# Performance work log

Hardware: AMD Instinct MI355X
Metric: run time of the kernel (lower is better)

## Reference

```python
import jax, jax.numpy as jnp
import numpy as np

B, N, D, H = 64, 1025, 768, 128

def setup_inputs() -> dict:
    key = jax.random.key(0)
    ks = jax.random.split(key, 5)
    x = jax.random.normal(ks[0], (B, N, D), dtype=jnp.float32)
    ln_w = jnp.ones((D,), dtype=jnp.float32)
    ln_b = jnp.zeros((D,), dtype=jnp.float32)
    w1 = jax.random.normal(ks[1], (D, H), dtype=jnp.float32) * (1.0 / np.sqrt(D))
    b1 = jnp.zeros((H,), dtype=jnp.float32)
    w2 = jax.random.normal(ks[2], (H, 1), dtype=jnp.float32) * (1.0 / np.sqrt(H))
    b2 = jnp.zeros((1,), dtype=jnp.float32)
    return {"x": x, "ln_w": ln_w, "ln_b": ln_b, "w1": w1, "b1": b1, "w2": w2, "b2": b2, "k": 256}

def _layernorm(x, w, b, eps=1e-5):
    mu = jnp.mean(x, axis=-1, keepdims=True)
    var = jnp.mean(jnp.square(x - mu), axis=-1, keepdims=True)
    return (x - mu) * jax.lax.rsqrt(var + eps) * w + b

def reference(x, ln_w, ln_b, w1, b1, w2, b2, k):
    Bb, Nn, Dd = x.shape
    h = _layernorm(x, ln_w, ln_b)                      # [B,N,D]
    h = jax.nn.gelu(h @ w1 + b1, approximate=False)    # [B,N,H] (torch GELU = exact erf)
    scores = (h @ w2 + b2).squeeze(-1)                 # [B,N]
    scores = scores.at[:, 0].set(1e9)                  # force CLS kept
    kk = min(k, Nn - 1)
    patch_scores = scores[:, 1:]                       # [B,N-1]
    _, topk_idx = jax.lax.top_k(patch_scores, kk)      # [B,k]
    topk_idx = topk_idx + 1
    cls_idx = jnp.zeros((Bb, 1), dtype=topk_idx.dtype)
    idx_full = jnp.concatenate([cls_idx, topk_idx], axis=1)  # [B,1+k]
    x_reduced = jnp.take_along_axis(x, idx_full[:, :, None], axis=1)  # [B,1+k,D]
    return (x_reduced, idx_full, scores)
```

## Files before the change

### kernel.cpp

```cpp
#include <hip/hip_runtime.h>
#include <hip/hip_bf16.h>
#include <math.h>

#define BB 64
#define NN 1025
#define DD 768
#define HH 128
#define KK 256
#define TOK (BB*NN)
#define OUT_XRED 0
#define OUT_IDX  (BB*(KK+1)*DD)
#define OUT_SC   (OUT_IDX + BB*(KK+1))

typedef float    f32x4 __attribute__((ext_vector_type(4)));
typedef __fp16   h16x2 __attribute__((ext_vector_type(2)));
typedef _Float16 f16x8 __attribute__((ext_vector_type(8)));
#define NSTEP (DD/32)

union U4F { uint4 u; f16x8 h; };
union H2U { h16x2 h; unsigned int u; };

__global__ __launch_bounds__(256) void k_cvtw(const float* __restrict__ w1,
                                              unsigned short* __restrict__ wt)
{
    int i = blockIdx.x*256 + threadIdx.x;
    int k = i >> 7, n = i & 127;
    union { _Float16 h; unsigned short s; } c;
    c.h = (_Float16)w1[i];
    int s = k >> 5, g = (k >> 3) & 3, j = k & 7;
    wt[((s*4 + g)*HH + n)*8 + j] = c.s;
}

__global__ __launch_bounds__(256) void k_fused(const float* __restrict__ x,
    const float* __restrict__ lnw, const float* __restrict__ lnb,
    const unsigned short* __restrict__ wt,
    const float* __restrict__ b1, const float* __restrict__ w2,
    const float* __restrict__ b2,
    float* __restrict__ scores_out)
{
    __shared__ uint4 planes[16*96];
    __shared__ float part[4][16];

    const int tid  = threadIdx.x;
    const int wave = tid >> 6, lane = tid & 63;
    const int g    = lane >> 4, t16 = lane & 15;
    const int t7   = t16 & 7;
    const int tok0 = blockIdx.x * 16;
    const int colbase = wave * 32;
    const int row = tid >> 4, l16 = tid & 15;

    const float4* srow4 = reinterpret_cast<const float4*>(x + (size_t)(tok0 + row) * DD);
    float4 xa[6], xb[6];
    float s_ = 0.f, ss = 0.f;
    #pragma unroll
    for (int j = 0; j < 6; ++j) {
        xa[j] = srow4[l16*2 + j*32];
        xb[j] = srow4[l16*2 + j*32 + 1];
        s_ += ((xa[j].x + xa[j].y) + (xa[j].z + xa[j].w))
            + ((xb[j].x + xb[j].y) + (xb[j].z + xb[j].w));
        ss += xa[j].x*xa[j].x + xa[j].y*xa[j].y + xa[j].z*xa[j].z + xa[j].w*xa[j].w
            + xb[j].x*xb[j].x + xb[j].y*xb[j].y + xb[j].z*xb[j].z + xb[j].w*xb[j].w;
    }
    #pragma unroll
    for (int m = 8; m; m >>= 1) { s_ += __shfl_xor(s_, m, 64); ss += __shfl_xor(ss, m, 64); }
    const float mu = s_ * (1.0f/768.0f);
    const float rs = 1.0f / sqrtf(ss * (1.0f/768.0f) - mu*mu + 1e-5f);

    const int rsz = row & 7;
    #pragma unroll
    for (int j = 0; j < 6; ++j) {
        float4 lw_a = reinterpret_cast<const float4*>(lnw)[l16*2 + j*32];
        float4 lw_b = reinterpret_cast<const float4*>(lnw)[l16*2 + j*32 + 1];
        float4 lb_a = reinterpret_cast<const float4*>(lnb)[l16*2 + j*32];
        float4 lb_b = reinterpret_cast<const float4*>(lnb)[l16*2 + j*32 + 1];
        H2U h01, h23, h45, h67;
        h01.h = __builtin_amdgcn_cvt_pkrtz((xa[j].x - mu)*rs*lw_a.x + lb_a.x,
                                           (xa[j].y - mu)*rs*lw_a.y + lb_a.y);
        h23.h = __builtin_amdgcn_cvt_pkrtz((xa[j].z - mu)*rs*lw_a.z + lb_a.z,
                                           (xa[j].w - mu)*rs*lw_a.w + lb_a.w);
        h45.h = __builtin_amdgcn_cvt_pkrtz((xb[j].x - mu)*rs*lw_b.x + lb_b.x,
                                           (xb[j].y - mu)*rs*lw_b.y + lb_b.y);
        h67.h = __builtin_amdgcn_cvt_pkrtz((xb[j].z - mu)*rs*lw_b.z + lb_b.z,
                                           (xb[j].w - mu)*rs*lw_b.w + lb_b.w);
        planes[row*96 + ((l16 + j*16) ^ rsz)] = make_uint4(h01.u, h23.u, h45.u, h67.u);
    }
    __syncthreads();

    const unsigned short* wtp = wt + ((size_t)g*HH + colbase + t16)*8;
    f32x4 acc0 = {0,0,0,0}, acc1 = {0,0,0,0};
    #pragma unroll 4
    for (int s = 0; s < NSTEP; ++s) {
        U4F Ah;
        Ah.u = planes[((s*4 + g) ^ t7) + t16*96];
        f16x8 B0 = *reinterpret_cast<const f16x8*>(wtp + (size_t)s*4096);
        f16x8 B1 = *reinterpret_cast<const f16x8*>(wtp + (size_t)s*4096 + 128);
        acc0 = __builtin_amdgcn_mfma_f32_16x16x32_f16(Ah.h, B0, acc0, 0, 0, 0);
        acc1 = __builtin_amdgcn_mfma_f32_16x16x32_f16(Ah.h, B1, acc1, 0, 0, 0);
    }

    const float b1A = b1[colbase + t16];
    const float b1B = b1[colbase + 16 + t16];
    const float w2A = w2[colbase + t16];
    const float w2B = w2[colbase + 16 + t16];
    const float is2 = 0.70710678f;

    float psum[4];
    #pragma unroll
    for (int r = 0; r < 4; ++r) {
        float v0 = acc0[r] + b1A;
        float v1 = acc1[r] + b1B;
        float g0 = 0.5f * v0 * (1.0f + erff(v0 * is2));
        float g1 = 0.5f * v1 * (1.0f + erff(v1 * is2));
        float p = g0 * w2A + g1 * w2B;
        #pragma unroll
        for (int m = 8; m; m >>= 1) p += __shfl_xor(p, m, 64);
        psum[r] = p;
    }
    if (t16 == 0) {
        #pragma unroll
        for (int r = 0; r < 4; ++r) part[wave][g*4 + r] = psum[r];
    }
    __syncthreads();
    if (tid < 16) {
        float s = part[0][tid] + part[1][tid] + part[2][tid] + part[3][tid] + b2[0];
        int tok = tok0 + tid;
        scores_out[tok] = ((tok % NN) == 0) ? 1.0e9f : s;
    }
}

__global__ __launch_bounds__(1024) void k_topk(const float* __restrict__ scores,
                                               float* __restrict__ idx_out)
{
    __shared__ float sk_[1024];
    __shared__ int   si[1024];
    const int tid = threadIdx.x;
    const int b   = blockIdx.x;
    sk_[tid] = scores[b*NN + 1 + tid];
    si[tid] = tid + 1;
    __syncthreads();
    for (int k = 2; k <= 1024; k <<= 1) {
        for (int j = k >> 1; j > 0; j >>= 1) {
            int ixj = tid ^ j;
            if (ixj > tid) {
                float sa = sk_[tid]; int ia = si[tid];
                float sb = sk_[ixj]; int ib = si[ixj];
                bool beforeB = (sb > sa) || (sb == sa && ib < ia);
                bool dirAsc  = ((tid & k) == 0);
                if (beforeB == dirAsc) {
                    sk_[tid] = sb; si[tid] = ib;
                    sk_[ixj] = sa; si[ixj] = ia;
                }
            }
            __syncthreads();
        }
    }
    if (tid == 0)  idx_out[b*(KK+1)] = 0.0f;
    if (tid < KK)  idx_out[b*(KK+1) + 1 + tid] = (float)si[tid];
}

__global__ __launch_bounds__(192) void k_gather(const float* __restrict__ x,
                                                const float* __restrict__ idx_out,
                                                float* __restrict__ xred)
{
    const int r = blockIdx.x;
    const int b = r / (KK+1);
    const int idx = (int)(idx_out[r] + 0.5f);
    const float4* src = reinterpret_cast<const float4*>(x + ((size_t)b*NN + idx) * DD);
    float4* dst = reinterpret_cast<float4*>(xred + (size_t)r * DD);
    dst[threadIdx.x] = src[threadIdx.x];
}

extern "C" void kernel_launch(void* const* d_in, const int* in_sizes, int n_in,
                              void* d_out, int out_size, void* d_ws, size_t ws_size,
                              hipStream_t stream)
{
    const float* x   = (const float*)d_in[0];
    const float* lnw = (const float*)d_in[1];
    const float* lnb = (const float*)d_in[2];
    const float* w1  = (const float*)d_in[3];
    const float* b1  = (const float*)d_in[4];
    const float* w2  = (const float*)d_in[5];
    const float* b2  = (const float*)d_in[6];

    float* out   = (float*)d_out;
    float* xred  = out + OUT_XRED;
    float* idxf  = out + OUT_IDX;
    float* scout = out + OUT_SC;

    unsigned short* wt = (unsigned short*)d_ws;

    k_cvtw  <<<DD*HH/256, 256, 0, stream>>>(w1, wt);
    k_fused <<<TOK/16, 256, 0, stream>>>(x, lnw, lnb, wt, b1, w2, b2, scout);
    k_topk  <<<BB, 1024, 0, stream>>>(scout, idxf);
    k_gather<<<BB*(KK+1), 192, 0, stream>>>(x, idxf, xred);
}
```

Measured before the change: 94.82 us.

## Fold LayerNorm affine into weights, prefetch B operands, fuse topk with gather

Folds the LayerNorm scale into the fp16 weights and precomputes per-column bias vectors. The GEMM can then consume raw x converted to fp16 in one pass, with mean and rstd applied afterward in the epilogue. This removes the second register-held pass over x and the lnw/lnb loads. It also software-prefetches the B fragments in a fully unrolled loop, sets an occupancy hint, and merges the gather into the top-k kernel, saving one launch at the cost of only 64 blocks doing the gather. Feeding un-normalized x to fp16 MFMA risks precision loss for large-mean rows, and the single-block cvec kernel adds a serial prologue.

```diff
diff --git a/kernel.cpp b/kernel.cpp
--- a/kernel.cpp
+++ b/kernel.cpp
@@ -21,24 +21,43 @@
 union H2U { h16x2 h; unsigned int u; };
 
 __global__ __launch_bounds__(256) void k_cvtw(const float* __restrict__ w1,
+                                              const float* __restrict__ lnw,
                                               unsigned short* __restrict__ wt)
 {
     int i = blockIdx.x*256 + threadIdx.x;
     int k = i >> 7, n = i & 127;
     union { _Float16 h; unsigned short s; } c;
-    c.h = (_Float16)w1[i];
+    c.h = (_Float16)(w1[i] * lnw[k]);
     int s = k >> 5, g = (k >> 3) & 3, j = k & 7;
     wt[((s*4 + g)*HH + n)*8 + j] = c.s;
 }
 
-__global__ __launch_bounds__(256) void k_fused(const float* __restrict__ x,
-    const float* __restrict__ lnw, const float* __restrict__ lnb,
+__global__ __launch_bounds__(128) void k_cvec(const float* __restrict__ w1,
+                                              const float* __restrict__ lnw,
+                                              const float* __restrict__ lnb,
+                                              const float* __restrict__ b1,
+                                              float* __restrict__ cvec)
+{
+    const int n = threadIdx.x;
+    float s1 = 0.f, s2 = 0.f;
+    #pragma unroll 8
+    for (int k = 0; k < DD; ++k) {
+        float wv = w1[k*HH + n];
+        s1 = fmaf(lnb[k], wv, s1);
+        s2 = fmaf(lnw[k], wv, s2);
+    }
+    cvec[n]      = s1 + b1[n];
+    cvec[128+n]  = s2;
+}
+
+__global__ __launch_bounds__(256, 6) void k_fused(const float* __restrict__ x,
     const unsigned short* __restrict__ wt,
-    const float* __restrict__ b1, const float* __restrict__ w2,
-    const float* __restrict__ b2,
+    const float* __restrict__ cvec,
+    const float* __restrict__ w2, const float* __restrict__ b2,
     float* __restrict__ scores_out)
 {
     __shared__ uint4 planes[16*96];
+    __shared__ float mus[16], rss[16];
     __shared__ float part[4][16];
 
     const int tid  = threadIdx.x;
@@ -50,65 +69,61 @@
     const int row = tid >> 4, l16 = tid & 15;
 
     const float4* srow4 = reinterpret_cast<const float4*>(x + (size_t)(tok0 + row) * DD);
-    float4 xa[6], xb[6];
+    const int rsz = row & 7;
     float s_ = 0.f, ss = 0.f;
     #pragma unroll
     for (int j = 0; j < 6; ++j) {
-        xa[j] = srow4[l16*2 + j*32];
-        xb[j] = srow4[l16*2 + j*32 + 1];
-        s_ += ((xa[j].x + xa[j].y) + (xa[j].z + xa[j].w))
-            + ((xb[j].x + xb[j].y) + (xb[j].z + xb[j].w));
-        ss += xa[j].x*xa[j].x + xa[j].y*xa[j].y + xa[j].z*xa[j].z + xa[j].w*xa[j].w
-            + xb[j].x*xb[j].x + xb[j].y*xb[j].y + xb[j].z*xb[j].z + xb[j].w*xb[j].w;
+        float4 a = srow4[l16*2 + j*32];
+        float4 b = srow4[l16*2 + j*32 + 1];
+        s_ += ((a.x + a.y) + (a.z + a.w)) + ((b.x + b.y) + (b.z + b.w));
+        ss += a.x*a.x + a.y*a.y + a.z*a.z + a.w*a.w
+            + b.x*b.x + b.y*b.y + b.z*b.z + b.w*b.w;
+        H2U h01, h23, h45, h67;
+        h01.h = __builtin_amdgcn_cvt_pkrtz(a.x, a.y);
+        h23.h = __builtin_amdgcn_cvt_pkrtz(a.z, a.w);
+        h45.h = __builtin_amdgcn_cvt_pkrtz(b.x, b.y);
+        h67.h = __builtin_amdgcn_cvt_pkrtz(b.z, b.w);
+        planes[row*96 + ((l16 + j*16) ^ rsz)] = make_uint4(h01.u, h23.u, h45.u, h67.u);
     }
     #pragma unroll
     for (int m = 8; m; m >>= 1) { s_ += __shfl_xor(s_, m, 64); ss += __shfl_xor(ss, m, 64); }
     const float mu = s_ * (1.0f/768.0f);
     const float rs = 1.0f / sqrtf(ss * (1.0f/768.0f) - mu*mu + 1e-5f);
-
-    const int rsz = row & 7;
-    #pragma unroll
-    for (int j = 0; j < 6; ++j) {
-        float4 lw_a = reinterpret_cast<const float4*>(lnw)[l16*2 + j*32];
-        float4 lw_b = reinterpret_cast<const float4*>(lnw)[l16*2 + j*32 + 1];
-        float4 lb_a = reinterpret_cast<const float4*>(lnb)[l16*2 + j*32];
-        float4 lb_b = reinterpret_cast<const float4*>(lnb)[l16*2 + j*32 + 1];
-        H2U h01, h23, h45, h67;
-        h01.h = __builtin_amdgcn_cvt_pkrtz((xa[j].x - mu)*rs*lw_a.x + lb_a.x,
-                                           (xa[j].y - mu)*rs*lw_a.y + lb_a.y);
-        h23.h = __builtin_amdgcn_cvt_pkrtz((xa[j].z - mu)*rs*lw_a.z + lb_a.z,
-                                           (xa[j].w - mu)*rs*lw_a.w + lb_a.w);
-        h45.h = __builtin_amdgcn_cvt_pkrtz((xb[j].x - mu)*rs*lw_b.x + lb_b.x,
-                                           (xb[j].y - mu)*rs*lw_b.y + lb_b.y);
-        h67.h = __builtin_amdgcn_cvt_pkrtz((xb[j].z - mu)*rs*lw_b.z + lb_b.z,
-                                           (xb[j].w - mu)*rs*lw_b.w + lb_b.w);
-        planes[row*96 + ((l16 + j*16) ^ rsz)] = make_uint4(h01.u, h23.u, h45.u, h67.u);
-    }
-    __syncthreads();
+    if (l16 == 0) { mus[row] = mu; rss[row] = rs; }
 
     const unsigned short* wtp = wt + ((size_t)g*HH + colbase + t16)*8;
+    f16x8 nB0 = *reinterpret_cast<const f16x8*>(wtp);
+    f16x8 nB1 = *reinterpret_cast<const f16x8*>(wtp + 128);
+
+    asm volatile("s_waitcnt lgkmcnt(0)" ::: "memory");
+    __builtin_amdgcn_s_barrier();
+
     f32x4 acc0 = {0,0,0,0}, acc1 = {0,0,0,0};
-    #pragma unroll 4
+    #pragma unroll
     for (int s = 0; s < NSTEP; ++s) {
+        f16x8 B0 = nB0, B1 = nB1;
+        if (s + 1 < NSTEP) {
+            nB0 = *reinterpret_cast<const f16x8*>(wtp + (size_t)(s+1)*4096);
+            nB1 = *reinterpret_cast<const f16x8*>(wtp + (size_t)(s+1)*4096 + 128);
+        }
         U4F Ah;
         Ah.u = planes[((s*4 + g) ^ t7) + t16*96];
-        f16x8 B0 = *reinterpret_cast<const f16x8*>(wtp + (size_t)s*4096);
-        f16x8 B1 = *reinterpret_cast<const f16x8*>(wtp + (size_t)s*4096 + 128);
         acc0 = __builtin_amdgcn_mfma_f32_16x16x32_f16(Ah.h, B0, acc0, 0, 0, 0);
         acc1 = __builtin_amdgcn_mfma_f32_16x16x32_f16(Ah.h, B1, acc1, 0, 0, 0);
     }
 
-    const float b1A = b1[colbase + t16];
-    const float b1B = b1[colbase + 16 + t16];
-    const float w2A = w2[colbase + t16];
-    const float w2B = w2[colbase + 16 + t16];
+    const int c0 = colbase + t16, c1i = colbase + 16 + t16;
+    const float c1A = cvec[c0],      c2A = cvec[128 + c0];
+    const float c1B = cvec[c1i],     c2B = cvec[128 + c1i];
+    const float w2A = w2[c0],        w2B = w2[c1i];
     const float is2 = 0.70710678f;
 
     float psum[4];
     #pragma unroll
     for (int r = 0; r < 4; ++r) {
-        float v0 = acc0[r] + b1A;
-        float v1 = acc1[r] + b1B;
+        const float mur = mus[g*4 + r], rsr = rss[g*4 + r];
+        float v0 = rsr*acc0[r] + c1A - mur*rsr*c2A;
+        float v1 = rsr*acc1[r] + c1B - mur*rsr*c2B;
         float g0 = 0.5f * v0 * (1.0f + erff(v0 * is2));
         float g1 = 0.5f * v1 * (1.0f + erff(v1 * is2));
         float p = g0 * w2A + g1 * w2B;
@@ -128,8 +143,10 @@
     }
 }
 
-__global__ __launch_bounds__(1024) void k_topk(const float* __restrict__ scores,
-                                               float* __restrict__ idx_out)
+__global__ __launch_bounds__(1024) void k_topk_gather(const float* __restrict__ scores,
+                                                      const float* __restrict__ x,
+                                                      float* __restrict__ idx_out,
+                                                      float* __restrict__ xred)
 {
     __shared__ float sk_[1024];
     __shared__ int   si[1024];
@@ -156,18 +173,14 @@
     }
     if (tid == 0)  idx_out[b*(KK+1)] = 0.0f;
     if (tid < KK)  idx_out[b*(KK+1) + 1 + tid] = (float)si[tid];
-}
-
-__global__ __launch_bounds__(192) void k_gather(const float* __restrict__ x,
-                                                const float* __restrict__ idx_out,
-                                                float* __restrict__ xred)
-{
-    const int r = blockIdx.x;
-    const int b = r / (KK+1);
-    const int idx = (int)(idx_out[r] + 0.5f);
-    const float4* src = reinterpret_cast<const float4*>(x + ((size_t)b*NN + idx) * DD);
-    float4* dst = reinterpret_cast<float4*>(xred + (size_t)r * DD);
-    dst[threadIdx.x] = src[threadIdx.x];
+
+    const float4* xb4 = reinterpret_cast<const float4*>(x + (size_t)b*NN*DD);
+    float4* dst4 = reinterpret_cast<float4*>(xred + (size_t)b*(KK+1)*DD);
+    for (int i = tid; i < (KK+1)*192; i += 1024) {
+        int r = i / 192, c = i - r*192;
+        int idx = (r == 0) ? 0 : si[r-1];
+        dst4[i] = xb4[idx*192 + c];
+    }
 }
 
 extern "C" void kernel_launch(void* const* d_in, const int* in_sizes, int n_in,
@@ -188,9 +201,10 @@
     float* scout = out + OUT_SC;
 
     unsigned short* wt = (unsigned short*)d_ws;
-
-    k_cvtw  <<<DD*HH/256, 256, 0, stream>>>(w1, wt);
-    k_fused <<<TOK/16, 256, 0, stream>>>(x, lnw, lnb, wt, b1, w2, b2, scout);
-    k_topk  <<<BB, 1024, 0, stream>>>(scout, idxf);
-    k_gather<<<BB*(KK+1), 192, 0, stream>>>(x, idxf, xred);
-}
+    float* cvec = (float*)((char*)d_ws + 196608);
+
+    k_cvtw <<<DD*HH/256, 256, 0, stream>>>(w1, lnw, wt);
+    k_cvec <<<1, 128, 0, stream>>>(w1, lnw, lnb, b1, cvec);
+    k_fused<<<TOK/16, 256, 0, stream>>>(x, wt, cvec, w2, b2, scout);
+    k_topk_gather<<<BB, 1024, 0, stream>>>(scout, x, idxf, xred);
+}
```

New measurement: 118.5 us. 24.9% more time.
